# Kernel tuning notes

Measured on AMD Instinct MI355X. Metric: run time of the kernel, lower is better.

## Reference

```python
import jax, jax.numpy as jnp
import numpy as np

B, N, H = 8, 256, 128  # graphs, nodes per graph (equal counts), hidden_dim


def setup_inputs() -> dict:
    key = jax.random.key(0)
    k1, k2, k3, k4, k5, k6 = jax.random.split(key, 6)
    total = B * N
    h = jax.random.normal(k1, (total, H), dtype=jnp.float32)
    pos = jax.random.normal(k2, (total, 3), dtype=jnp.float32)
    # sorted segment ids, equal counts per graph (padding becomes a reshape)
    batch = jnp.repeat(jnp.arange(B, dtype=jnp.int64), N)
    # phi: Linear(2H+1 -> H) -> SiLU -> Linear(H -> 1), torch default init
    s1 = 1.0 / np.sqrt(2 * H + 1)
    s2 = 1.0 / np.sqrt(H)
    W1 = jax.random.uniform(k3, (2 * H + 1, H), minval=-s1, maxval=s1, dtype=jnp.float32)
    b1 = jax.random.uniform(k4, (H,), minval=-s1, maxval=s1, dtype=jnp.float32)
    W2 = jax.random.uniform(k5, (H, 1), minval=-s2, maxval=s2, dtype=jnp.float32)
    b2 = jax.random.uniform(k6, (1,), minval=-s2, maxval=s2, dtype=jnp.float32)
    return {"h": h, "pos": pos, "batch": batch, "W1": W1, "b1": b1, "W2": W2, "b2": b2}


def _safe_norm(diff):
    # exact forward (0 on diagonal), grad-safe (no nan from sqrt at 0)
    sq = jnp.sum(diff * diff, axis=-1, keepdims=True)
    pos_sq = sq > 0
    return jnp.where(pos_sq, jnp.sqrt(jnp.where(pos_sq, sq, 1.0)), 0.0)


def reference(h, pos, batch, W1, b1, W2, b2):
    # batch is sorted with equal counts per graph -> padding == reshape,
    # mask is all-True, so v_pred_padded[mask] == reshape back to [total, 3].
    hp = h.reshape(B, N, H)
    pp = pos.reshape(B, N, 3)

    # diff[b, p, q] = pos[b, q] - pos[b, p]  (matches unsqueeze(1) - unsqueeze(2))
    diff = pp[:, None, :, :] - pp[:, :, None, :]        # [B, N, N, 3]
    dist = _safe_norm(diff)                              # [B, N, N, 1]

    # cat([h_i, h_j, dist]) @ W1 done without materializing the concat:
    # h_i[b,p,q] = h[b,q], h_j[b,p,q] = h[b,p]
    Wa, Wb, wd = W1[:H], W1[H:2 * H], W1[2 * H]
    pre = (hp @ Wa)[:, None, :, :] + (hp @ Wb)[:, :, None, :] + dist * wd + b1
    coeff = jax.nn.silu(pre) @ W2 + b2                   # [B, N, N, 1]

    v = jnp.sum(coeff * diff, axis=2)                    # [B, N, 3]
    return v.reshape(B * N, 3)
```

## Files before the change

### kernel.cpp

```cpp
#include <hip/hip_runtime.h>
#include <math.h>

#define BATCH 8
#define NPTS  256
#define HDIM  128
#define TOTAL (BATCH * NPTS)

#define NEG_LOG2E -1.4426950408889634f
#define NEG_LN2   -0.6931471805599453f

__global__ __launch_bounds__(HDIM) void evh_prep_kernel(
    const float* __restrict__ h, const float* __restrict__ W1,
    const float* __restrict__ b1, const float* __restrict__ W2,
    float* __restrict__ A_T4, float* __restrict__ Bb,
    float* __restrict__ wdx, float* __restrict__ w2x,
    float* __restrict__ out)
{
    __shared__ float hrow[HDIM];
    const int t = blockIdx.x;
    const int c = threadIdx.x;
    hrow[c] = h[t * HDIM + c];
    if (t == 0) {
        wdx[c] = W1[2 * HDIM * HDIM + c] * NEG_LOG2E;
        w2x[c] = W2[c] * NEG_LN2;
    }
    if (c < 3) out[t * 3 + c] = 0.f;
    __syncthreads();

    float a = 0.f, bsum = 0.f;
#pragma unroll 8
    for (int k = 0; k < HDIM; ++k) {
        const float hv = hrow[k];
        a    = fmaf(hv, W1[k * HDIM + c], a);
        bsum = fmaf(hv, W1[(HDIM + k) * HDIM + c], bsum);
    }
    A_T4[(c >> 2) * (4 * TOTAL) + 4 * t + (c & 3)] = a * NEG_LOG2E;
    Bb[t * HDIM + c] = (bsum + b1[c]) * NEG_LOG2E;
}

__global__ __launch_bounds__(256) void evh_pair_kernel(
    const float* __restrict__ A_T4, const float* __restrict__ Bb,
    const float* __restrict__ wdx, const float* __restrict__ w2x,
    const float* __restrict__ pos, const float* __restrict__ b2,
    float* __restrict__ out)
{
    const int blk = blockIdx.x;
    const int ch  = blk & 1;
    const int b   = blk >> 8;
    const int i0  = ((blk >> 1) & 127) * 2;
    const int tid = threadIdx.x;
    const int brow  = b * NPTS;
    const int row_j = brow + tid;

    const float pjx = pos[row_j * 3 + 0];
    const float pjy = pos[row_j * 3 + 1];
    const float pjz = pos[row_j * 3 + 2];

    float dx0, dy0, dz0, dist0, dx1, dy1, dz1, dist1;
    {
        const int r0 = brow + i0, r1 = r0 + 1;
        dx0 = pjx - pos[r0 * 3 + 0];
        dy0 = pjy - pos[r0 * 3 + 1];
        dz0 = pjz - pos[r0 * 3 + 2];
        dist0 = sqrtf(dx0 * dx0 + dy0 * dy0 + dz0 * dz0);
        dx1 = pjx - pos[r1 * 3 + 0];
        dy1 = pjy - pos[r1 * 3 + 1];
        dz1 = pjz - pos[r1 * 3 + 2];
        dist1 = sqrtf(dx1 * dx1 + dy1 * dy1 + dz1 * dz1);
    }

    const float* __restrict__ bb0p = Bb + (size_t)(brow + i0) * HDIM + ch * 64;
    const float* __restrict__ bb1p = bb0p + HDIM;
    const float* __restrict__ wdp  = wdx + ch * 64;
    const float* __restrict__ w2p  = w2x + ch * 64;
    const float* __restrict__ ap   = A_T4 + 4 * row_j
                                     + (size_t)(ch * 16) * (4 * TOTAL);

    float acc0 = 0.f, acc1 = 0.f;

#define CELL(AK, BK, WDK, W2K, ACC, D)                                  \
    {                                                                   \
        const float pre2 = fmaf((D), (WDK), (AK) + (BK));               \
        const float e = __builtin_amdgcn_exp2f(pre2);                   \
        const float r = __builtin_amdgcn_rcpf(1.f + e);                 \
        ACC = fmaf((W2K), pre2 * r, ACC);                               \
    }

#pragma unroll 4
    for (int q = 0; q < 16; ++q) {
        const float4 a  = *reinterpret_cast<const float4*>(
                              ap + (size_t)q * (4 * TOTAL));
        const float4 b0 = *reinterpret_cast<const float4*>(bb0p + 4 * q);
        const float4 b1 = *reinterpret_cast<const float4*>(bb1p + 4 * q);
        const float4 wd = *reinterpret_cast<const float4*>(wdp + 4 * q);
        const float4 w2 = *reinterpret_cast<const float4*>(w2p + 4 * q);

        CELL(a.x, b0.x, wd.x, w2.x, acc0, dist0)
        CELL(a.y, b0.y, wd.y, w2.y, acc0, dist0)
        CELL(a.z, b0.z, wd.z, w2.z, acc0, dist0)
        CELL(a.w, b0.w, wd.w, w2.w, acc0, dist0)
        CELL(a.x, b1.x, wd.x, w2.x, acc1, dist1)
        CELL(a.y, b1.y, wd.y, w2.y, acc1, dist1)
        CELL(a.z, b1.z, wd.z, w2.z, acc1, dist1)
        CELL(a.w, b1.w, wd.w, w2.w, acc1, dist1)
    }
#undef CELL

    const float cext = (ch == 0) ? b2[0] : 0.f;
    const int wave = tid >> 6;
    const int lane = tid & 63;

    const float c0 = acc0 + cext;
    const float c1 = acc1 + cext;
    float v0x = c0 * dx0, v0y = c0 * dy0, v0z = c0 * dz0;
    float v1x = c1 * dx1, v1y = c1 * dy1, v1z = c1 * dz1;
#pragma unroll
    for (int off = 32; off >= 1; off >>= 1) {
        v0x += __shfl_xor(v0x, off, 64);
        v0y += __shfl_xor(v0y, off, 64);
        v0z += __shfl_xor(v0z, off, 64);
        v1x += __shfl_xor(v1x, off, 64);
        v1y += __shfl_xor(v1y, off, 64);
        v1z += __shfl_xor(v1z, off, 64);
    }

    __shared__ float vsh[4][6];
    if (lane == 0) {
        vsh[wave][0] = v0x; vsh[wave][1] = v0y; vsh[wave][2] = v0z;
        vsh[wave][3] = v1x; vsh[wave][4] = v1y; vsh[wave][5] = v1z;
    }
    __syncthreads();
    if (tid < 6) {
        const float val = vsh[0][tid] + vsh[1][tid] + vsh[2][tid] + vsh[3][tid];
        const int s = tid / 3, comp = tid % 3;
        atomicAdd(&out[(brow + i0 + s) * 3 + comp], val);
    }
}

extern "C" void kernel_launch(void* const* d_in, const int* in_sizes, int n_in,
                              void* d_out, int out_size, void* d_ws, size_t ws_size,
                              hipStream_t stream) {
    const float* h   = (const float*)d_in[0];
    const float* pos = (const float*)d_in[1];
    const float* W1  = (const float*)d_in[3];
    const float* b1  = (const float*)d_in[4];
    const float* W2  = (const float*)d_in[5];
    const float* b2  = (const float*)d_in[6];
    float* out = (float*)d_out;

    float* A_T4 = (float*)d_ws;
    float* Bb   = A_T4 + TOTAL * HDIM;
    float* wdx  = Bb + TOTAL * HDIM;
    float* w2x  = wdx + HDIM;

    evh_prep_kernel<<<TOTAL, HDIM, 0, stream>>>(h, W1, b1, W2,
                                                A_T4, Bb, wdx, w2x, out);
    evh_pair_kernel<<<TOTAL, 256, 0, stream>>>(A_T4, Bb, wdx, w2x,
                                               pos, b2, out);
}
```

Baseline: 33.67 us.

## Split hidden dim across four blocks and use packed float2 math in pair kernel

The pair kernel now splits the 128-wide hidden dimension into four 32-wide chunks instead of two, which quadruples the grid and adds more atomic adds per output. The per-element silu-weighted accumulation is rewritten with two-wide vector types so the compiler can emit packed FMA/add/mul instructions. The A loads are batched four at a time to expose memory-level parallelism, and launch bounds now request four blocks per CU. The cost is twice as many atomics and reductions, with less work per block to amortize the pos loads, shuffles and shared-memory reduction.

```diff
diff --git a/kernel.cpp b/kernel.cpp
--- a/kernel.cpp
+++ b/kernel.cpp
@@ -8,6 +8,8 @@
 
 #define NEG_LOG2E -1.4426950408889634f
 #define NEG_LN2   -0.6931471805599453f
+
+typedef float f2 __attribute__((ext_vector_type(2)));
 
 __global__ __launch_bounds__(HDIM) void evh_prep_kernel(
     const float* __restrict__ h, const float* __restrict__ W1,
@@ -38,16 +40,16 @@
     Bb[t * HDIM + c] = (bsum + b1[c]) * NEG_LOG2E;
 }
 
-__global__ __launch_bounds__(256) void evh_pair_kernel(
+__global__ __launch_bounds__(256, 4) void evh_pair_kernel(
     const float* __restrict__ A_T4, const float* __restrict__ Bb,
     const float* __restrict__ wdx, const float* __restrict__ w2x,
     const float* __restrict__ pos, const float* __restrict__ b2,
     float* __restrict__ out)
 {
     const int blk = blockIdx.x;
-    const int ch  = blk & 1;
-    const int b   = blk >> 8;
-    const int i0  = ((blk >> 1) & 127) * 2;
+    const int ch  = blk & 3;
+    const int b   = blk >> 9;
+    const int i0  = ((blk >> 2) & 127) * 2;
     const int tid = threadIdx.x;
     const int brow  = b * NPTS;
     const int row_j = brow + tid;
@@ -56,62 +58,76 @@
     const float pjy = pos[row_j * 3 + 1];
     const float pjz = pos[row_j * 3 + 2];
 
-    float dx0, dy0, dz0, dist0, dx1, dy1, dz1, dist1;
+    float dx0, dy0, dz0, dx1, dy1, dz1;
+    f2 d0, d1;
     {
         const int r0 = brow + i0, r1 = r0 + 1;
         dx0 = pjx - pos[r0 * 3 + 0];
         dy0 = pjy - pos[r0 * 3 + 1];
         dz0 = pjz - pos[r0 * 3 + 2];
-        dist0 = sqrtf(dx0 * dx0 + dy0 * dy0 + dz0 * dz0);
+        const float t0 = sqrtf(dx0 * dx0 + dy0 * dy0 + dz0 * dz0);
+        d0.x = t0; d0.y = t0;
         dx1 = pjx - pos[r1 * 3 + 0];
         dy1 = pjy - pos[r1 * 3 + 1];
         dz1 = pjz - pos[r1 * 3 + 2];
-        dist1 = sqrtf(dx1 * dx1 + dy1 * dy1 + dz1 * dz1);
+        const float t1 = sqrtf(dx1 * dx1 + dy1 * dy1 + dz1 * dz1);
+        d1.x = t1; d1.y = t1;
     }
 
-    const float* __restrict__ bb0p = Bb + (size_t)(brow + i0) * HDIM + ch * 64;
+    const float* __restrict__ bb0p = Bb + (size_t)(brow + i0) * HDIM + ch * 32;
     const float* __restrict__ bb1p = bb0p + HDIM;
-    const float* __restrict__ wdp  = wdx + ch * 64;
-    const float* __restrict__ w2p  = w2x + ch * 64;
+    const float* __restrict__ wdp  = wdx + ch * 32;
+    const float* __restrict__ w2p  = w2x + ch * 32;
     const float* __restrict__ ap   = A_T4 + 4 * row_j
-                                     + (size_t)(ch * 16) * (4 * TOTAL);
+                                     + (size_t)(ch * 8) * (4 * TOTAL);
 
-    float acc0 = 0.f, acc1 = 0.f;
+    f2 acc0 = {0.f, 0.f}, acc1 = {0.f, 0.f};
 
-#define CELL(AK, BK, WDK, W2K, ACC, D)                                  \
+#define PAIR(A2, B2, WD2, W22, ACC, DIST2)                              \
     {                                                                   \
-        const float pre2 = fmaf((D), (WDK), (AK) + (BK));               \
-        const float e = __builtin_amdgcn_exp2f(pre2);                   \
-        const float r = __builtin_amdgcn_rcpf(1.f + e);                 \
-        ACC = fmaf((W2K), pre2 * r, ACC);                               \
+        const f2 t = __builtin_elementwise_fma((DIST2), (WD2), (A2) + (B2)); \
+        f2 e; e.x = __builtin_amdgcn_exp2f(t.x);                        \
+              e.y = __builtin_amdgcn_exp2f(t.y);                        \
+        const f2 dpl = e + 1.0f;                                        \
+        f2 r; r.x = __builtin_amdgcn_rcpf(dpl.x);                       \
+              r.y = __builtin_amdgcn_rcpf(dpl.y);                       \
+        ACC = __builtin_elementwise_fma((W22) * t, r, ACC);             \
     }
 
-#pragma unroll 4
-    for (int q = 0; q < 16; ++q) {
-        const float4 a  = *reinterpret_cast<const float4*>(
-                              ap + (size_t)q * (4 * TOTAL));
-        const float4 b0 = *reinterpret_cast<const float4*>(bb0p + 4 * q);
-        const float4 b1 = *reinterpret_cast<const float4*>(bb1p + 4 * q);
-        const float4 wd = *reinterpret_cast<const float4*>(wdp + 4 * q);
-        const float4 w2 = *reinterpret_cast<const float4*>(w2p + 4 * q);
+#pragma unroll
+    for (int g = 0; g < 2; ++g) {
+        float4 a[4];
+#pragma unroll
+        for (int q = 0; q < 4; ++q)
+            a[q] = *reinterpret_cast<const float4*>(
+                       ap + (size_t)(g * 4 + q) * (4 * TOTAL));
+#pragma unroll
+        for (int q = 0; q < 4; ++q) {
+            const int qq = g * 4 + q;
+            const float4 b0 = *reinterpret_cast<const float4*>(bb0p + 4 * qq);
+            const float4 b1 = *reinterpret_cast<const float4*>(bb1p + 4 * qq);
+            const float4 wd = *reinterpret_cast<const float4*>(wdp + 4 * qq);
+            const float4 w2 = *reinterpret_cast<const float4*>(w2p + 4 * qq);
+            const f2 alo = {a[q].x, a[q].y}, ahi = {a[q].z, a[q].w};
+            const f2 b0lo = {b0.x, b0.y},   b0hi = {b0.z, b0.w};
+            const f2 b1lo = {b1.x, b1.y},   b1hi = {b1.z, b1.w};
+            const f2 wdlo = {wd.x, wd.y},   wdhi = {wd.z, wd.w};
+            const f2 w2lo = {w2.x, w2.y},   w2hi = {w2.z, w2.w};
 
-        CELL(a.x, b0.x, wd.x, w2.x, acc0, dist0)
-        CELL(a.y, b0.y, wd.y, w2.y, acc0, dist0)
-        CELL(a.z, b0.z, wd.z, w2.z, acc0, dist0)
-        CELL(a.w, b0.w, wd.w, w2.w, acc0, dist0)
-        CELL(a.x, b1.x, wd.x, w2.x, acc1, dist1)
-        CELL(a.y, b1.y, wd.y, w2.y, acc1, dist1)
-        CELL(a.z, b1.z, wd.z, w2.z, acc1, dist1)
-        CELL(a.w, b1.w, wd.w, w2.w, acc1, dist1)
+            PAIR(alo, b0lo, wdlo, w2lo, acc0, d0)
+            PAIR(ahi, b0hi, wdhi, w2hi, acc0, d0)
+            PAIR(alo, b1lo, wdlo, w2lo, acc1, d1)
+            PAIR(ahi, b1hi, wdhi, w2hi, acc1, d1)
+        }
     }
-#undef CELL
+#undef PAIR
 
     const float cext = (ch == 0) ? b2[0] : 0.f;
     const int wave = tid >> 6;
     const int lane = tid & 63;
 
-    const float c0 = acc0 + cext;
-    const float c1 = acc1 + cext;
+    const float c0 = acc0.x + acc0.y + cext;
+    const float c1 = acc1.x + acc1.y + cext;
     float v0x = c0 * dx0, v0y = c0 * dy0, v0z = c0 * dz0;
     float v1x = c1 * dx1, v1y = c1 * dy1, v1z = c1 * dz1;
 #pragma unroll
@@ -155,6 +171,6 @@
 
     evh_prep_kernel<<<TOTAL, HDIM, 0, stream>>>(h, W1, b1, W2,
                                                 A_T4, Bb, wdx, w2x, out);
-    evh_pair_kernel<<<TOTAL, 256, 0, stream>>>(A_T4, Bb, wdx, w2x,
-                                               pos, b2, out);
+    evh_pair_kernel<<<4 * TOTAL, 256, 0, stream>>>(A_T4, Bb, wdx, w2x,
+                                                   pos, b2, out);
 }
```

New measurement: 53.32 us. 1.58x slower.

## Tile pair kernel over four i-rows and four hidden-dim chunks, caching A in registers

Applied to the files above, without the earlier changes.

Each block of the pair kernel now handles four output rows i and a quarter of the hidden dimension, where before it handled two rows and half. The per-thread A slice (32 values) is loaded once into registers and reused across the four rows. This cuts global A traffic per pair while keeping the grid size the same. The costs are higher register pressure from the 32-float A array and more atomics per output element (four chunks instead of two).

```diff
diff --git a/kernel.cpp b/kernel.cpp
--- a/kernel.cpp
+++ b/kernel.cpp
@@ -5,6 +5,8 @@
 #define NPTS  256
 #define HDIM  128
 #define TOTAL (BATCH * NPTS)
+#define IT    4
+#define QCH   32
 
 #define NEG_LOG2E -1.4426950408889634f
 #define NEG_LN2   -0.6931471805599453f
@@ -45,9 +47,10 @@
     float* __restrict__ out)
 {
     const int blk = blockIdx.x;
-    const int ch  = blk & 1;
+    const int ch  = blk & 3;
+    const int ig  = (blk >> 2) & 63;
     const int b   = blk >> 8;
-    const int i0  = ((blk >> 1) & 127) * 2;
+    const int i0  = ig * IT;
     const int tid = threadIdx.x;
     const int brow  = b * NPTS;
     const int row_j = brow + tid;
@@ -56,27 +59,28 @@
     const float pjy = pos[row_j * 3 + 1];
     const float pjz = pos[row_j * 3 + 2];
 
-    float dx0, dy0, dz0, dist0, dx1, dy1, dz1, dist1;
-    {
-        const int r0 = brow + i0, r1 = r0 + 1;
-        dx0 = pjx - pos[r0 * 3 + 0];
-        dy0 = pjy - pos[r0 * 3 + 1];
-        dz0 = pjz - pos[r0 * 3 + 2];
-        dist0 = sqrtf(dx0 * dx0 + dy0 * dy0 + dz0 * dz0);
-        dx1 = pjx - pos[r1 * 3 + 0];
-        dy1 = pjy - pos[r1 * 3 + 1];
-        dz1 = pjz - pos[r1 * 3 + 2];
-        dist1 = sqrtf(dx1 * dx1 + dy1 * dy1 + dz1 * dz1);
+    float dx[IT], dy[IT], dz[IT], dist[IT];
+#pragma unroll
+    for (int s = 0; s < IT; ++s) {
+        const int ri = brow + i0 + s;
+        dx[s] = pjx - pos[ri * 3 + 0];
+        dy[s] = pjy - pos[ri * 3 + 1];
+        dz[s] = pjz - pos[ri * 3 + 2];
+        dist[s] = sqrtf(dx[s] * dx[s] + dy[s] * dy[s] + dz[s] * dz[s]);
     }
 
-    const float* __restrict__ bb0p = Bb + (size_t)(brow + i0) * HDIM + ch * 64;
-    const float* __restrict__ bb1p = bb0p + HDIM;
-    const float* __restrict__ wdp  = wdx + ch * 64;
-    const float* __restrict__ w2p  = w2x + ch * 64;
-    const float* __restrict__ ap   = A_T4 + 4 * row_j
-                                     + (size_t)(ch * 16) * (4 * TOTAL);
+    const float* __restrict__ ap = A_T4 + 4 * row_j
+                                   + (size_t)(ch * 8) * (4 * TOTAL);
+    float4 a[8];
+#pragma unroll
+    for (int q = 0; q < 8; ++q)
+        a[q] = *reinterpret_cast<const float4*>(ap + (size_t)q * (4 * TOTAL));
 
-    float acc0 = 0.f, acc1 = 0.f;
+    const float* __restrict__ bbp = Bb + (size_t)(brow + i0) * HDIM + ch * QCH;
+    const float* __restrict__ wdp = wdx + ch * QCH;
+    const float* __restrict__ w2p = w2x + ch * QCH;
+
+    float acc[IT] = {0.f, 0.f, 0.f, 0.f};
 
 #define CELL(AK, BK, WDK, W2K, ACC, D)                                  \
     {                                                                   \
@@ -86,23 +90,19 @@
         ACC = fmaf((W2K), pre2 * r, ACC);                               \
     }
 
-#pragma unroll 4
-    for (int q = 0; q < 16; ++q) {
-        const float4 a  = *reinterpret_cast<const float4*>(
-                              ap + (size_t)q * (4 * TOTAL));
-        const float4 b0 = *reinterpret_cast<const float4*>(bb0p + 4 * q);
-        const float4 b1 = *reinterpret_cast<const float4*>(bb1p + 4 * q);
+#pragma unroll
+    for (int q = 0; q < 8; ++q) {
         const float4 wd = *reinterpret_cast<const float4*>(wdp + 4 * q);
         const float4 w2 = *reinterpret_cast<const float4*>(w2p + 4 * q);
-
-        CELL(a.x, b0.x, wd.x, w2.x, acc0, dist0)
-        CELL(a.y, b0.y, wd.y, w2.y, acc0, dist0)
-        CELL(a.z, b0.z, wd.z, w2.z, acc0, dist0)
-        CELL(a.w, b0.w, wd.w, w2.w, acc0, dist0)
-        CELL(a.x, b1.x, wd.x, w2.x, acc1, dist1)
-        CELL(a.y, b1.y, wd.y, w2.y, acc1, dist1)
-        CELL(a.z, b1.z, wd.z, w2.z, acc1, dist1)
-        CELL(a.w, b1.w, wd.w, w2.w, acc1, dist1)
+#pragma unroll
+        for (int s = 0; s < IT; ++s) {
+            const float4 bb = *reinterpret_cast<const float4*>(
+                                  bbp + (size_t)s * HDIM + 4 * q);
+            CELL(a[q].x, bb.x, wd.x, w2.x, acc[s], dist[s])
+            CELL(a[q].y, bb.y, wd.y, w2.y, acc[s], dist[s])
+            CELL(a[q].z, bb.z, wd.z, w2.z, acc[s], dist[s])
+            CELL(a[q].w, bb.w, wd.w, w2.w, acc[s], dist[s])
+        }
     }
 #undef CELL
 
@@ -110,27 +110,35 @@
     const int wave = tid >> 6;
     const int lane = tid & 63;
 
-    const float c0 = acc0 + cext;
-    const float c1 = acc1 + cext;
-    float v0x = c0 * dx0, v0y = c0 * dy0, v0z = c0 * dz0;
-    float v1x = c1 * dx1, v1y = c1 * dy1, v1z = c1 * dz1;
+    float v[IT][3];
+#pragma unroll
+    for (int s = 0; s < IT; ++s) {
+        const float co = acc[s] + cext;
+        v[s][0] = co * dx[s];
+        v[s][1] = co * dy[s];
+        v[s][2] = co * dz[s];
+    }
 #pragma unroll
     for (int off = 32; off >= 1; off >>= 1) {
-        v0x += __shfl_xor(v0x, off, 64);
-        v0y += __shfl_xor(v0y, off, 64);
-        v0z += __shfl_xor(v0z, off, 64);
-        v1x += __shfl_xor(v1x, off, 64);
-        v1y += __shfl_xor(v1y, off, 64);
-        v1z += __shfl_xor(v1z, off, 64);
+#pragma unroll
+        for (int s = 0; s < IT; ++s) {
+            v[s][0] += __shfl_xor(v[s][0], off, 64);
+            v[s][1] += __shfl_xor(v[s][1], off, 64);
+            v[s][2] += __shfl_xor(v[s][2], off, 64);
+        }
     }
 
-    __shared__ float vsh[4][6];
+    __shared__ float vsh[4][IT * 3];
     if (lane == 0) {
-        vsh[wave][0] = v0x; vsh[wave][1] = v0y; vsh[wave][2] = v0z;
-        vsh[wave][3] = v1x; vsh[wave][4] = v1y; vsh[wave][5] = v1z;
+#pragma unroll
+        for (int s = 0; s < IT; ++s) {
+            vsh[wave][s * 3 + 0] = v[s][0];
+            vsh[wave][s * 3 + 1] = v[s][1];
+            vsh[wave][s * 3 + 2] = v[s][2];
+        }
     }
     __syncthreads();
-    if (tid < 6) {
+    if (tid < IT * 3) {
         const float val = vsh[0][tid] + vsh[1][tid] + vsh[2][tid] + vsh[3][tid];
         const int s = tid / 3, comp = tid % 3;
         atomicAdd(&out[(brow + i0 + s) * 3 + comp], val);
@@ -155,6 +163,6 @@
 
     evh_prep_kernel<<<TOTAL, HDIM, 0, stream>>>(h, W1, b1, W2,
                                                 A_T4, Bb, wdx, w2x, out);
-    evh_pair_kernel<<<TOTAL, 256, 0, stream>>>(A_T4, Bb, wdx, w2x,
-                                               pos, b2, out);
+    evh_pair_kernel<<<BATCH * (NPTS / IT) * 4, 256, 0, stream>>>(
+        A_T4, Bb, wdx, w2x, pos, b2, out);
 }
```

New measurement: 39.13 us. +16.2%, slower.

## Switch pair-kernel SiLU math and intermediates to packed fp16

Applied to the files above, without the earlier changes.

The precomputed projections, weights and the per-pair SiLU evaluation move from fp32 to packed half2 arithmetic, with exp2 and rcp done on half2. Partial sums are accumulated in fp16 per group of eight channels and then promoted to fp32. Halving the workspace bytes and using packed math is meant to cut both the transcendental throughput cost and the memory traffic of the pair kernel. The risk is accuracy loss from fp16 rounding and range limits on the pre-activations and accumulations. Launch bounds also gain an occupancy hint of eight blocks.

```diff
diff --git a/kernel.cpp b/kernel.cpp
--- a/kernel.cpp
+++ b/kernel.cpp
@@ -1,4 +1,5 @@
 #include <hip/hip_runtime.h>
+#include <hip/hip_fp16.h>
 #include <math.h>
 
 #define BATCH 8
@@ -12,8 +13,8 @@
 __global__ __launch_bounds__(HDIM) void evh_prep_kernel(
     const float* __restrict__ h, const float* __restrict__ W1,
     const float* __restrict__ b1, const float* __restrict__ W2,
-    float* __restrict__ A_T4, float* __restrict__ Bb,
-    float* __restrict__ wdx, float* __restrict__ w2x,
+    __half* __restrict__ A_h, __half* __restrict__ Bbh,
+    __half* __restrict__ wdh, __half* __restrict__ w2h,
     float* __restrict__ out)
 {
     __shared__ float hrow[HDIM];
@@ -21,8 +22,8 @@
     const int c = threadIdx.x;
     hrow[c] = h[t * HDIM + c];
     if (t == 0) {
-        wdx[c] = W1[2 * HDIM * HDIM + c] * NEG_LOG2E;
-        w2x[c] = W2[c] * NEG_LN2;
+        wdh[c] = __float2half_rn(W1[2 * HDIM * HDIM + c] * NEG_LOG2E);
+        w2h[c] = __float2half_rn(W2[c] * NEG_LN2);
     }
     if (c < 3) out[t * 3 + c] = 0.f;
     __syncthreads();
@@ -34,13 +35,14 @@
         a    = fmaf(hv, W1[k * HDIM + c], a);
         bsum = fmaf(hv, W1[(HDIM + k) * HDIM + c], bsum);
     }
-    A_T4[(c >> 2) * (4 * TOTAL) + 4 * t + (c & 3)] = a * NEG_LOG2E;
-    Bb[t * HDIM + c] = (bsum + b1[c]) * NEG_LOG2E;
+    A_h[((size_t)(c >> 3) * TOTAL + t) * 8 + (c & 7)] =
+        __float2half_rn(a * NEG_LOG2E);
+    Bbh[(size_t)t * HDIM + c] = __float2half_rn((bsum + b1[c]) * NEG_LOG2E);
 }
 
-__global__ __launch_bounds__(256) void evh_pair_kernel(
-    const float* __restrict__ A_T4, const float* __restrict__ Bb,
-    const float* __restrict__ wdx, const float* __restrict__ w2x,
+__global__ __launch_bounds__(256, 8) void evh_pair_kernel(
+    const __half* __restrict__ A_h, const __half* __restrict__ Bbh,
+    const __half* __restrict__ wdh, const __half* __restrict__ w2h,
     const float* __restrict__ pos, const float* __restrict__ b2,
     float* __restrict__ out)
 {
@@ -68,50 +70,50 @@
         dz1 = pjz - pos[r1 * 3 + 2];
         dist1 = sqrtf(dx1 * dx1 + dy1 * dy1 + dz1 * dz1);
     }
+    const __half2 dd0 = __float2half2_rn(dist0);
+    const __half2 dd1 = __float2half2_rn(dist1);
+    const __half2 one2 = __float2half2_rn(1.0f);
+    const __half2 zero2 = __float2half2_rn(0.0f);
 
-    const float* __restrict__ bb0p = Bb + (size_t)(brow + i0) * HDIM + ch * 64;
-    const float* __restrict__ bb1p = bb0p + HDIM;
-    const float* __restrict__ wdp  = wdx + ch * 64;
-    const float* __restrict__ w2p  = w2x + ch * 64;
-    const float* __restrict__ ap   = A_T4 + 4 * row_j
-                                     + (size_t)(ch * 16) * (4 * TOTAL);
+    const __half* __restrict__ bb0p = Bbh + (size_t)(brow + i0) * HDIM + ch * 64;
+    const __half* __restrict__ bb1p = bb0p + HDIM;
+    const __half* __restrict__ wdp  = wdh + ch * 64;
+    const __half* __restrict__ w2p  = w2h + ch * 64;
+    const __half* __restrict__ ap   = A_h + ((size_t)(ch * 8) * TOTAL + row_j) * 8;
 
-    float acc0 = 0.f, acc1 = 0.f;
+    float accf0 = 0.f, accf1 = 0.f;
 
-#define CELL(AK, BK, WDK, W2K, ACC, D)                                  \
-    {                                                                   \
-        const float pre2 = fmaf((D), (WDK), (AK) + (BK));               \
-        const float e = __builtin_amdgcn_exp2f(pre2);                   \
-        const float r = __builtin_amdgcn_rcpf(1.f + e);                 \
-        ACC = fmaf((W2K), pre2 * r, ACC);                               \
+    union V { uint4 u; __half2 h[4]; };
+
+#pragma unroll
+    for (int g = 0; g < 8; ++g) {
+        V a, b0, b1, wd, w2;
+        a.u  = *reinterpret_cast<const uint4*>(ap + (size_t)g * TOTAL * 8);
+        b0.u = *reinterpret_cast<const uint4*>(bb0p + 8 * g);
+        b1.u = *reinterpret_cast<const uint4*>(bb1p + 8 * g);
+        wd.u = *reinterpret_cast<const uint4*>(wdp + 8 * g);
+        w2.u = *reinterpret_cast<const uint4*>(w2p + 8 * g);
+
+        __half2 s0 = zero2, s1 = zero2;
+#pragma unroll
+        for (int k = 0; k < 4; ++k) {
+            const __half2 t0 = __hfma2(dd0, wd.h[k], __hadd2(a.h[k], b0.h[k]));
+            const __half2 t1 = __hfma2(dd1, wd.h[k], __hadd2(a.h[k], b1.h[k]));
+            const __half2 r0 = h2rcp(__hadd2(h2exp2(t0), one2));
+            const __half2 r1 = h2rcp(__hadd2(h2exp2(t1), one2));
+            s0 = __hfma2(__hmul2(w2.h[k], t0), r0, s0);
+            s1 = __hfma2(__hmul2(w2.h[k], t1), r1, s1);
+        }
+        accf0 += __low2float(s0) + __high2float(s0);
+        accf1 += __low2float(s1) + __high2float(s1);
     }
-
-#pragma unroll 4
-    for (int q = 0; q < 16; ++q) {
-        const float4 a  = *reinterpret_cast<const float4*>(
-                              ap + (size_t)q * (4 * TOTAL));
-        const float4 b0 = *reinterpret_cast<const float4*>(bb0p + 4 * q);
-        const float4 b1 = *reinterpret_cast<const float4*>(bb1p + 4 * q);
-        const float4 wd = *reinterpret_cast<const float4*>(wdp + 4 * q);
-        const float4 w2 = *reinterpret_cast<const float4*>(w2p + 4 * q);
-
-        CELL(a.x, b0.x, wd.x, w2.x, acc0, dist0)
-        CELL(a.y, b0.y, wd.y, w2.y, acc0, dist0)
-        CELL(a.z, b0.z, wd.z, w2.z, acc0, dist0)
-        CELL(a.w, b0.w, wd.w, w2.w, acc0, dist0)
-        CELL(a.x, b1.x, wd.x, w2.x, acc1, dist1)
-        CELL(a.y, b1.y, wd.y, w2.y, acc1, dist1)
-        CELL(a.z, b1.z, wd.z, w2.z, acc1, dist1)
-        CELL(a.w, b1.w, wd.w, w2.w, acc1, dist1)
-    }
-#undef CELL
 
     const float cext = (ch == 0) ? b2[0] : 0.f;
     const int wave = tid >> 6;
     const int lane = tid & 63;
 
-    const float c0 = acc0 + cext;
-    const float c1 = acc1 + cext;
+    const float c0 = accf0 + cext;
+    const float c1 = accf1 + cext;
     float v0x = c0 * dx0, v0y = c0 * dy0, v0z = c0 * dz0;
     float v1x = c1 * dx1, v1y = c1 * dy1, v1z = c1 * dz1;
 #pragma unroll
@@ -148,13 +150,13 @@
     const float* b2  = (const float*)d_in[6];
     float* out = (float*)d_out;
 
-    float* A_T4 = (float*)d_ws;
-    float* Bb   = A_T4 + TOTAL * HDIM;
-    float* wdx  = Bb + TOTAL * HDIM;
-    float* w2x  = wdx + HDIM;
+    __half* A_h = (__half*)d_ws;
+    __half* Bbh = A_h + (size_t)TOTAL * HDIM;
+    __half* wdh = Bbh + (size_t)TOTAL * HDIM;
+    __half* w2h = wdh + HDIM;
 
     evh_prep_kernel<<<TOTAL, HDIM, 0, stream>>>(h, W1, b1, W2,
-                                                A_T4, Bb, wdx, w2x, out);
-    evh_pair_kernel<<<TOTAL, 256, 0, stream>>>(A_T4, Bb, wdx, w2x,
+                                                A_h, Bbh, wdh, w2h, out);
+    evh_pair_kernel<<<TOTAL, 256, 0, stream>>>(A_h, Bbh, wdh, w2h,
                                                pos, b2, out);
 }
```

Result: slower. 39.82 us (+18.3%).
